# Performance work log

Hardware: AMD Instinct MI355X
Metric: run time of the kernel (lower is better)

The kernel has to match this reference:

```python
import jax, jax.numpy as jnp
import numpy as np

N, C, H, W = 8, 256, 100, 252
TOPK_RATIO = 0.1
CLUSTER_RATIO = 0.125
KNN_K = 10


def setup_inputs() -> dict:
    key = jax.random.key(0)
    ks = jax.random.split(key, 4)
    x = jax.random.normal(ks[0], (N, C, H, W), jnp.float32)
    w1 = jax.random.normal(ks[1], (C, C), jnp.float32) * (1.0 / np.sqrt(C))
    b1 = jnp.zeros((C,), jnp.float32)
    w2 = jax.random.normal(ks[2], (C,), jnp.float32) * (1.0 / np.sqrt(C))
    b2 = jnp.zeros((1,), jnp.float32)
    dis_priority = jnp.ones((N, H, W), jnp.float32)
    record_len = jnp.array([4, 4], dtype=jnp.int32)
    return {"x": x, "w1": w1, "b1": b1, "w2": w2, "b2": b2,
            "dis_priority": dis_priority, "record_len": record_len}


def _layernorm(t, eps=1e-5):
    mu = jnp.mean(t, -1, keepdims=True)
    var = jnp.var(t, -1, keepdims=True)
    return (t - mu) / jnp.sqrt(var + eps)


def reference(x, w1, b1, w2, b2, dis_priority, record_len):
    HW = H * W
    S = int(HW * TOPK_RATIO)                       # sampled tokens per CAV
    K = max(int(np.ceil(S * CLUSTER_RATIO)), 1)    # DPC-KNN cluster count

    xf = x.reshape(N, C, HW)
    # SortSampler: 2layer-fc-256 score net (1x1 convs == per-pixel MLP)
    h1 = jax.nn.relu(jnp.einsum('nch,dc->ndh', xf, w1) + b1[None, :, None])
    score = jax.nn.sigmoid(jnp.einsum('nch,c->nh', h1, w2) + b2)   # [N,HW]
    score = score * dis_priority.reshape(N, HW)

    conf_topk, topk_idx = jax.lax.top_k(score, S)  # descending-sort top-k
    tokens = jnp.take_along_axis(xf, topk_idx[:, None, :], axis=2)  # [N,C,S]
    tokens = _layernorm(tokens.transpose(0, 2, 1))                  # [N,S,C]
    tokens = tokens * conf_topk[..., None]

    # --- cluster_dpc_knn (TCFormer-style DPC-KNN) ---
    sq = jnp.sum(tokens * tokens, -1)
    d2 = sq[:, :, None] + sq[:, None, :] - 2.0 * jnp.einsum('bsc,btc->bst', tokens, tokens)
    dist = jnp.sqrt(jnp.maximum(d2, 1e-12)) / np.sqrt(C)            # [N,S,S]
    neg_near, _ = jax.lax.top_k(-dist, KNN_K)                       # k nearest
    density = jnp.exp(-jnp.mean(neg_near * neg_near, -1))
    density = density + jax.random.uniform(jax.random.key(1), density.shape) * 1e-6
    mask = density[:, None, :] > density[:, :, None]
    dist_max = dist.max(axis=(1, 2), keepdims=True)
    parent_dist = jnp.where(mask, dist, dist_max).min(-1)           # [N,S]
    cscore = parent_dist * density
    _, index_down = jax.lax.top_k(cscore, K)                        # [N,K]
    dist_c = jnp.take_along_axis(dist, index_down[:, :, None], axis=1)  # [N,K,S]
    idx_cluster = jnp.argmin(dist_c, axis=1)                        # [N,S]
    bidx = jnp.arange(N)[:, None]
    idx_cluster = idx_cluster.at[bidx, index_down].set(jnp.arange(K)[None, :])

    # --- merge_tokens: confidence-weighted average per cluster ---
    flat_idx = (idx_cluster + jnp.arange(N)[:, None] * K).reshape(-1)
    wgt = conf_topk.reshape(-1)
    all_w = jax.ops.segment_sum(wgt, flat_idx, num_segments=N * K) + 1e-6
    norm_w = (wgt / all_w[flat_idx])[:, None]
    merged = jax.ops.segment_sum(tokens.reshape(-1, C) * norm_w, flat_idx,
                                 num_segments=N * K).reshape(N, K, C)

    # index_points: broadcast cluster token back to its members
    src = jnp.take_along_axis(merged, idx_cluster[..., None], axis=1)  # [N,S,C]

    # scatter sampled tokens into dense spatial grid
    out = jnp.zeros((N, C, HW), x.dtype)
    out = out.at[bidx, :, topk_idx].set(src)       # [N,S] adv idx -> [N,S,C]

    # ego CAV (first in each record group) keeps full-resolution features
    starts = jnp.concatenate([jnp.zeros((1,), jnp.int32),
                              jnp.cumsum(record_len)[:-1].astype(jnp.int32)])
    is_ego = jnp.zeros((N,), bool).at[starts].set(True)
    out = jnp.where(is_ego[:, None, None], xf, out)
    return out.reshape(N, C, H, W)
```

## Files before the change

kernel.cpp:

```cpp
#include <hip/hip_runtime.h>
#include <cstdio>
#include <cstdint>

#define NN  8
#define CCH 256
#define HWP 25200
#define SS  2520
#define KCL 315
#define KNN 10

__device__ __forceinline__ unsigned fmap(float f) {
  unsigned u = __float_as_uint(f);
  return (u & 0x80000000u) ? ~u : (u | 0x80000000u);
}
__device__ __forceinline__ float funmap(unsigned u) {
  unsigned b = (u & 0x80000000u) ? (u & 0x7fffffffu) : ~u;
  return __uint_as_float(b);
}

__global__ __launch_bounds__(256) void k_w1t(const float* __restrict__ w1, float* __restrict__ w1T) {
  __shared__ float tile[32][33];
  const int bx = blockIdx.x * 32, by = blockIdx.y * 32;
  const int tx = threadIdx.x, ty = threadIdx.y;
  for (int r = 0; r < 32; r += 8)
    tile[ty + r][tx] = w1[(by + ty + r) * CCH + bx + tx];
  __syncthreads();
  for (int r = 0; r < 32; r += 8)
    w1T[(bx + ty + r) * CCH + by + tx] = tile[tx][ty + r];
}

__global__ __launch_bounds__(256) void k_score(
    const float* __restrict__ x, const float* __restrict__ w1T,
    const float* __restrict__ b1, const float* __restrict__ w2,
    const float* __restrict__ b2, const float* __restrict__ pri,
    float* __restrict__ scores)
{
  __shared__ float Wl[16 * 256];
  __shared__ float Xl[16 * 64];
  __shared__ float red[64 * 33];
  const int n = blockIdx.y, p0 = blockIdx.x * 64, tid = threadIdx.x;
  const int dt = tid & 31, pt = tid >> 5;
  const int skk = tid >> 4, sq = tid & 15;
  int sgp = p0 + 4 * sq; if (sgp > HWP - 4) sgp = HWP - 4;
  float acc[8][8];
#pragma unroll
  for (int i = 0; i < 8; ++i)
#pragma unroll
    for (int j = 0; j < 8; ++j) acc[i][j] = 0.f;

  float4 wreg[4], xreg;
  {
    const float4* src = (const float4*)w1T;
#pragma unroll
    for (int i = 0; i < 4; ++i) wreg[i] = src[tid + 256 * i];
    xreg = *(const float4*)&x[(size_t)(n * CCH + skk) * HWP + sgp];
  }

  for (int c0 = 0; c0 < CCH; c0 += 16) {
    __syncthreads();
    {
      float4* dst = (float4*)Wl;
#pragma unroll
      for (int i = 0; i < 4; ++i) dst[tid + 256 * i] = wreg[i];
      *(float4*)&Xl[skk * 64 + 4 * sq] = xreg;
    }
    if (c0 + 16 < CCH) {
      const float4* src = (const float4*)(w1T + (size_t)(c0 + 16) * CCH);
#pragma unroll
      for (int i = 0; i < 4; ++i) wreg[i] = src[tid + 256 * i];
      xreg = *(const float4*)&x[(size_t)(n * CCH + c0 + 16 + skk) * HWP + sgp];
    }
    __syncthreads();
#pragma unroll
    for (int kk = 0; kk < 16; ++kk) {
      const float4 w0 = *(const float4*)&Wl[kk * 256 + 4 * dt];
      const float4 w1v = *(const float4*)&Wl[kk * 256 + 128 + 4 * dt];
      const float4 x0 = *(const float4*)&Xl[kk * 64 + 4 * pt];
      const float4 x1 = *(const float4*)&Xl[kk * 64 + 32 + 4 * pt];
      const float a[8] = {w0.x, w0.y, w0.z, w0.w, w1v.x, w1v.y, w1v.z, w1v.w};
      const float b[8] = {x0.x, x0.y, x0.z, x0.w, x1.x, x1.y, x1.z, x1.w};
#pragma unroll
      for (int di = 0; di < 8; ++di)
#pragma unroll
        for (int pj = 0; pj < 8; ++pj) acc[di][pj] += a[di] * b[pj];
    }
  }
  __syncthreads();
  float part[8];
#pragma unroll
  for (int pj = 0; pj < 8; ++pj) part[pj] = 0.f;
#pragma unroll
  for (int di = 0; di < 8; ++di) {
    int d = (di < 4) ? (4 * dt + di) : (128 + 4 * dt + di - 4);
    float bb = b1[d], wv = w2[d];
#pragma unroll
    for (int pj = 0; pj < 8; ++pj) {
      float h = acc[di][pj] + bb; h = h > 0.f ? h : 0.f;
      part[pj] += h * wv;
    }
  }
#pragma unroll
  for (int pj = 0; pj < 8; ++pj) {
    int px = (pj < 4) ? (4 * pt + pj) : (32 + 4 * pt + pj - 4);
    red[px * 33 + dt] = part[pj];
  }
  __syncthreads();
  if (tid < 64) {
    float s = b2[0];
#pragma unroll
    for (int g = 0; g < 32; ++g) s += red[tid * 33 + g];
    float sc = 1.f / (1.f + expf(-s));
    int p = p0 + tid;
    if (p < HWP) scores[n * HWP + p] = sc * pri[n * HWP + p];
  }
}

__device__ __forceinline__ void bitonic4096_desc(unsigned long long* keys, int tid) {
  for (int k = 2; k <= 4096; k <<= 1) {
    for (int j = k >> 1; j > 0; j >>= 1) {
      for (int i = tid; i < 4096; i += 1024) {
        int ixj = i ^ j;
        if (ixj > i) {
          unsigned long long a = keys[i], b = keys[ixj];
          bool up = ((i & k) == 0);
          if ((a < b) == up) { keys[i] = b; keys[ixj] = a; }
        }
      }
      __syncthreads();
    }
  }
}

__global__ __launch_bounds__(1024) void k_topk_sample(
    const float* __restrict__ scores, int* __restrict__ topk_idx, float* __restrict__ conf)
{
  __shared__ unsigned long long keys[4096];
  unsigned* hist = (unsigned*)keys;
  __shared__ unsigned sh_rank, sh_chosen;
  __shared__ int sh_cnt;
  const int n = blockIdx.x;
  const int tid = threadIdx.x;
  const int sub = tid & 15;
  if (tid == 0) sh_rank = SS;
  __syncthreads();
  unsigned prefix = 0, pmask = 0;
  for (int shift = 24; shift >= 0; shift -= 8) {
    for (int b = tid; b < 4096; b += 1024) hist[b] = 0;
    __syncthreads();
    for (int e4 = tid; e4 < HWP / 4; e4 += 1024) {
      float4 v = *(const float4*)&scores[n * HWP + 4 * e4];
      const float vv[4] = {v.x, v.y, v.z, v.w};
#pragma unroll
      for (int j = 0; j < 4; ++j) {
        unsigned u = fmap(vv[j]);
        if ((u & pmask) == prefix) atomicAdd(&hist[(((u >> shift) & 255u) << 4) + sub], 1u);
      }
    }
    __syncthreads();
    if (tid < 256) {
      unsigned s = 0;
#pragma unroll
      for (int j = 0; j < 16; ++j) s += hist[(tid << 4) + j];
      __syncthreads();
      hist[tid << 4] = s;
    } else __syncthreads();
    __syncthreads();
    if (tid == 0) {
      unsigned r = sh_rank, chosen = 0;
      for (int b = 255; b >= 0; --b) {
        unsigned cb = hist[b << 4];
        if (cb < r) r -= cb; else { chosen = (unsigned)b; break; }
      }
      sh_rank = r; sh_chosen = chosen;
    }
    __syncthreads();
    prefix |= sh_chosen << shift;
    pmask  |= 0xFFu << shift;
    __syncthreads();
  }
  const unsigned uT = prefix;
  if (tid == 0) sh_cnt = 0;
  __syncthreads();
  for (int i = tid; i < 4096; i += 1024) keys[i] = 0ULL;
  __syncthreads();
  for (int e4 = tid; e4 < HWP / 4; e4 += 1024) {
    float4 v = *(const float4*)&scores[n * HWP + 4 * e4];
    const float vv[4] = {v.x, v.y, v.z, v.w};
#pragma unroll
    for (int j = 0; j < 4; ++j) {
      unsigned u = fmap(vv[j]);
      if (u >= uT) {
        int s = atomicAdd(&sh_cnt, 1);
        if (s < 4096) keys[s] = ((unsigned long long)u << 32) | (unsigned)(~(unsigned)(4 * e4 + j));
      }
    }
  }
  __syncthreads();
  bitonic4096_desc(keys, tid);
  for (int t = tid; t < SS; t += 1024) {
    unsigned long long kv = keys[t];
    topk_idx[n * SS + t] = (int)(~(unsigned)kv);
    conf[n * SS + t] = funmap((unsigned)(kv >> 32));
  }
}

__device__ __forceinline__ float block_sum256(float v, float* scratch) {
#pragma unroll
  for (int o = 32; o > 0; o >>= 1) v += __shfl_down(v, o);
  int wid = threadIdx.x >> 6, lane = threadIdx.x & 63;
  if (lane == 0) scratch[wid] = v;
  __syncthreads();
  float r = scratch[0] + scratch[1] + scratch[2] + scratch[3];
  __syncthreads();
  return r;
}

__global__ __launch_bounds__(256) void k_gather_ln(
    const float* __restrict__ x, const int* __restrict__ topk_idx,
    const float* __restrict__ conf, float* __restrict__ tokens, float* __restrict__ sq)
{
  __shared__ float scratch[4];
  const int t = blockIdx.x, n = blockIdx.y, c = threadIdx.x;
  const int p = topk_idx[n * SS + t];
  float v = x[(size_t)(n * CCH + c) * HWP + p];
  float mu = block_sum256(v, scratch) * (1.f / CCH);
  float d = v - mu;
  float var = block_sum256(d * d, scratch) * (1.f / CCH);
  float inv = 1.f / sqrtf(var + 1e-5f);
  float tok = d * inv * conf[n * SS + t];
  tokens[(size_t)(n * SS + t) * CCH + c] = tok;
  float s2 = block_sum256(tok * tok, scratch);
  if (c == 0) sq[n * SS + t] = s2;
}

__global__ __launch_bounds__(256) void k_ttrans(
    const float* __restrict__ tokens, float* __restrict__ tokensT)
{
  __shared__ float tile[64][68];
  const int n = blockIdx.z, t0 = blockIdx.x * 64, cc0 = blockIdx.y * 64;
  const int tid = threadIdx.x;
  for (int l = tid; l < 1024; l += 256) {
    int tr = l >> 4, q = l & 15;
    int gt = t0 + tr;
    float4 v = {0.f, 0.f, 0.f, 0.f};
    if (gt < SS) v = *(const float4*)&tokens[(size_t)(n * SS + gt) * CCH + cc0 + 4 * q];
    *(float4*)&tile[tr][4 * q] = v;
  }
  __syncthreads();
  for (int l = tid; l < 1024; l += 256) {
    int cr = l >> 4, q = l & 15;
    int gt = t0 + 4 * q;
    if (gt <= SS - 4) {
      float4 v;
      v.x = tile[4 * q + 0][cr]; v.y = tile[4 * q + 1][cr];
      v.z = tile[4 * q + 2][cr]; v.w = tile[4 * q + 3][cr];
      *(float4*)&tokensT[(size_t)(n * CCH + cc0 + cr) * SS + gt] = v;
    }
  }
}

__global__ __launch_bounds__(256) void k_gram(
    const float* __restrict__ tokensT, const float* __restrict__ sq,
    float* __restrict__ d2, int* __restrict__ d2max)
{
  const int bi = blockIdx.y, bj = blockIdx.x, n = blockIdx.z;
  if (bj < bi) return;
  __shared__ float Al[16 * 128], Bl[16 * 128];
  __shared__ float redm[256];
  const int i0 = bi * 128, j0 = bj * 128, tid = threadIdx.x;
  const int ti = tid & 15, tj = tid >> 4;
  float acc[8][8];
#pragma unroll
  for (int i = 0; i < 8; ++i)
#pragma unroll
    for (int j = 0; j < 8; ++j) acc[i][j] = 0.f;

  float4 areg[2], breg[2];
  auto stage_load = [&](int c0) {
#pragma unroll
    for (int l0 = 0; l0 < 2; ++l0) {
      int l = tid + 256 * l0;
      int kk = l >> 5, q = l & 31;
      size_t srow = (size_t)(n * CCH + c0 + kk) * SS;
      float4 z = {0.f, 0.f, 0.f, 0.f};
      int gi = i0 + 4 * q;
      areg[l0] = (gi <= SS - 4) ? *(const float4*)&tokensT[srow + gi] : z;
      int gj = j0 + 4 * q;
      breg[l0] = (gj <= SS - 4) ? *(const float4*)&tokensT[srow + gj] : z;
    }
  };
  stage_load(0);

  for (int c0 = 0; c0 < CCH; c0 += 16) {
    __syncthreads();
#pragma unroll
    for (int l0 = 0; l0 < 2; ++l0) {
      int l = tid + 256 * l0;
      int kk = l >> 5, q = l & 31;
      *(float4*)&Al[kk * 128 + 4 * q] = areg[l0];
      *(float4*)&Bl[kk * 128 + 4 * q] = breg[l0];
    }
    if (c0 + 16 < CCH) stage_load(c0 + 16);
    __syncthreads();
#pragma unroll
    for (int kk = 0; kk < 16; ++kk) {
      const float4 a0 = *(const float4*)&Al[kk * 128 + 4 * ti];
      const float4 a1 = *(const float4*)&Al[kk * 128 + 64 + 4 * ti];
      const float4 b0 = *(const float4*)&Bl[kk * 128 + 4 * tj];
      const float4 b1 = *(const float4*)&Bl[kk * 128 + 64 + 4 * tj];
      const float a[8] = {a0.x, a0.y, a0.z, a0.w, a1.x, a1.y, a1.z, a1.w};
      const float b[8] = {b0.x, b0.y, b0.z, b0.w, b1.x, b1.y, b1.z, b1.w};
#pragma unroll
      for (int ii = 0; ii < 8; ++ii)
#pragma unroll
        for (int jj = 0; jj < 8; ++jj) acc[ii][jj] += a[ii] * b[jj];
    }
  }
  int gi[8], gj[8];
  float sqi[8], sqj[8];
#pragma unroll
  for (int ii = 0; ii < 8; ++ii) {
    gi[ii] = i0 + ((ii < 4) ? (4 * ti + ii) : (64 + 4 * ti + ii - 4));
    sqi[ii] = (gi[ii] < SS) ? sq[n * SS + gi[ii]] : 0.f;
    gj[ii] = j0 + ((ii < 4) ? (4 * tj + ii) : (64 + 4 * tj + ii - 4));
    sqj[ii] = (gj[ii] < SS) ? sq[n * SS + gj[ii]] : 0.f;
  }
  float outv[8][8];
  float mx = -3e38f;
#pragma unroll
  for (int ii = 0; ii < 8; ++ii)
#pragma unroll
    for (int jj = 0; jj < 8; ++jj) {
      float o = sqi[ii] + sqj[jj] - 2.f * acc[ii][jj];
      outv[ii][jj] = o;
      if (gi[ii] < SS && gj[jj] < SS) mx = fmaxf(mx, o);
    }
#pragma unroll
  for (int ii = 0; ii < 8; ++ii) {
    if (gi[ii] < SS) {
      size_t row = (size_t)(n * SS + gi[ii]) * SS;
      int jb0 = j0 + 4 * tj;
      float4 o0 = {outv[ii][0], outv[ii][1], outv[ii][2], outv[ii][3]};
      *(float4*)&d2[row + jb0] = o0;
      int jb1 = j0 + 64 + 4 * tj;
      if (jb1 < SS) {
        float4 o1 = {outv[ii][4], outv[ii][5], outv[ii][6], outv[ii][7]};
        *(float4*)&d2[row + jb1] = o1;
      }
    }
  }
  if (bi != bj) {
#pragma unroll
    for (int jj = 0; jj < 8; ++jj) {
      if (gj[jj] < SS) {
        size_t row = (size_t)(n * SS + gj[jj]) * SS;
        int ib0 = i0 + 4 * ti;
        float4 m0 = {outv[0][jj], outv[1][jj], outv[2][jj], outv[3][jj]};
        *(float4*)&d2[row + ib0] = m0;
        int ib1 = i0 + 64 + 4 * ti;
        if (ib1 < SS) {
          float4 m1 = {outv[4][jj], outv[5][jj], outv[6][jj], outv[7][jj]};
          *(float4*)&d2[row + ib1] = m1;
        }
      }
    }
  }
  redm[tid] = mx; __syncthreads();
  for (int s = 128; s > 0; s >>= 1) {
    if (tid < s) redm[tid] = fmaxf(redm[tid], redm[tid + s]);
    __syncthreads();
  }
  if (tid == 0) atomicMax(&d2max[n], __float_as_int(redm[0]));
}

__global__ __launch_bounds__(256) void k_knn(
    const float* __restrict__ d2, float* __restrict__ density)
{
  const int n = blockIdx.y;
  const int w = threadIdx.x >> 6, lane = threadIdx.x & 63;
  const int i = blockIdx.x * 4 + w;
  const float* dr = &d2[(size_t)(n * SS + i) * SS];
  float s[KNN];
#pragma unroll
  for (int k = 0; k < KNN; ++k) s[k] = 3e38f;
  for (int e = lane; e < SS; e += 64) {
    float t = dr[e];
#pragma unroll
    for (int k = 0; k < KNN; ++k) {
      float lo = fminf(s[k], t);
      t = fmaxf(s[k], t);
      s[k] = lo;
    }
  }
  float sum = 0.f;
  for (int r = 0; r < KNN; ++r) {
    float m = s[0];
#pragma unroll
    for (int o = 32; o > 0; o >>= 1) m = fminf(m, __shfl_xor(m, o));
    unsigned long long msk = __ballot(s[0] == m);
    int first = __ffsll(msk) - 1;
    if (lane == first) {
#pragma unroll
      for (int k = 0; k < KNN - 1; ++k) s[k] = s[k + 1];
      s[KNN - 1] = 3e38f;
    }
    sum += fmaxf(m, 1e-12f);
  }
  if (lane == 0) density[n * SS + i] = expf(-sum * (1.f / (KNN * CCH)));
}

__global__ __launch_bounds__(256) void k_parent(
    const float* __restrict__ d2, const float* __restrict__ density,
    const int* __restrict__ d2max, float* __restrict__ cscore)
{
  __shared__ float swv[4];
  const int i = blockIdx.x, n = blockIdx.y, tid = threadIdx.x;
  const float di = density[n * SS + i];
  const float* dr = &d2[(size_t)(n * SS + i) * SS];
  float m = 3e38f;
  for (int e = tid; e < SS; e += 256) {
    float dj = density[n * SS + e];
    float v = dr[e];
    if (dj > di && v < m) m = v;
  }
#pragma unroll
  for (int o = 32; o > 0; o >>= 1) m = fminf(m, __shfl_down(m, o));
  int wid = tid >> 6, lane = tid & 63;
  if (lane == 0) swv[wid] = m;
  __syncthreads();
  if (tid == 0) {
    float mm = fminf(fminf(swv[0], swv[1]), fminf(swv[2], swv[3]));
    mm = fminf(mm, __int_as_float(d2max[n]));
    float pd = sqrtf(fmaxf(mm, 1e-12f)) * 0.0625f;
    cscore[n * SS + i] = pd * di;
  }
}

__global__ __launch_bounds__(1024) void k_topk_centers(
    const float* __restrict__ cscore, int* __restrict__ index_down)
{
  __shared__ unsigned long long keys[4096];
  const int n = blockIdx.x, tid = threadIdx.x;
  for (int i = tid; i < 4096; i += 1024) {
    unsigned long long kv = 0ULL;
    if (i < SS) kv = ((unsigned long long)fmap(cscore[n * SS + i]) << 32) | (unsigned)(~(unsigned)i);
    keys[i] = kv;
  }
  __syncthreads();
  bitonic4096_desc(keys, tid);
  for (int t = tid; t < KCL; t += 1024)
    index_down[n * KCL + t] = (int)(~(unsigned)keys[t]);
}

__global__ __launch_bounds__(256) void k_assign(
    const float* __restrict__ d2, const int* __restrict__ index_down,
    int* __restrict__ idx_cluster)
{
  const int n = blockIdx.y;
  const int i = blockIdx.x * 256 + threadIdx.x;
  if (i >= SS) return;
  float best = 3e38f; int bk = 0;
  for (int k = 0; k < KCL; ++k) {
    int r = index_down[n * KCL + k];
    float v = d2[(size_t)(n * SS + r) * SS + i];
    if (v < best) { best = v; bk = k; }
  }
  idx_cluster[n * SS + i] = bk;
}

__global__ void k_center_overwrite(const int* __restrict__ index_down, int* __restrict__ idx_cluster) {
  const int n = blockIdx.x; const int k = threadIdx.x;
  if (k < KCL) idx_cluster[n * SS + index_down[n * KCL + k]] = k;
}

__global__ __launch_bounds__(256) void k_weights(
    const int* __restrict__ idx_cluster, const float* __restrict__ conf, float* __restrict__ all_w)
{
  const int n = blockIdx.y; const int i = blockIdx.x * 256 + threadIdx.x;
  if (i >= SS) return;
  atomicAdd(&all_w[n * KCL + idx_cluster[n * SS + i]], conf[n * SS + i]);
}

__global__ __launch_bounds__(256) void k_merge(
    const int* __restrict__ idx_cluster, const float* __restrict__ conf,
    const float* __restrict__ all_w, const float* __restrict__ tokens, float* __restrict__ merged)
{
  const int t = blockIdx.x, n = blockIdx.y, c = threadIdx.x;
  const int k = idx_cluster[n * SS + t];
  const float w = conf[n * SS + t] / (all_w[n * KCL + k] + 1e-6f);
  atomicAdd(&merged[(size_t)(n * KCL + k) * CCH + c],
            tokens[(size_t)(n * SS + t) * CCH + c] * w);
}

__global__ __launch_bounds__(256) void k_kmap(
    const int* __restrict__ topk_idx, const int* __restrict__ idx_cluster, int* __restrict__ kmap)
{
  const int n = blockIdx.y; const int i = blockIdx.x * 256 + threadIdx.x;
  if (i >= SS) return;
  kmap[n * HWP + topk_idx[n * SS + i]] = idx_cluster[n * SS + i];
}

__global__ void k_ego(const int* __restrict__ record_len, int R, int* __restrict__ ego) {
  if (threadIdx.x == 0 && blockIdx.x == 0) {
    int acc = 0;
    for (int r = 0; r < R; ++r) {
      if (acc >= 0 && acc < NN) ego[acc] = 1;
      acc += record_len[r];
    }
  }
}

__global__ __launch_bounds__(256) void k_output(
    const float* __restrict__ x, const float* __restrict__ merged,
    const int* __restrict__ kmap, const int* __restrict__ ego, float* __restrict__ out)
{
  const int n = blockIdx.z;
  const int cg = blockIdx.y * 16;
  const int p4 = blockIdx.x * 256 + threadIdx.x;
  if (p4 >= HWP / 4) return;
  const size_t pbase = 4 * (size_t)p4;
  if (ego[n]) {
#pragma unroll 4
    for (int c = cg; c < cg + 16; ++c) {
      const size_t base = (size_t)(n * CCH + c) * HWP + pbase;
      *(float4*)&out[base] = *(const float4*)&x[base];
    }
  } else {
    const int4 k4 = *(const int4*)&kmap[n * HWP + pbase];
    const float* mb = &merged[(size_t)n * KCL * CCH];
#pragma unroll 4
    for (int c = cg; c < cg + 16; ++c) {
      float4 v;
      v.x = (k4.x >= 0) ? mb[k4.x * CCH + c] : 0.f;
      v.y = (k4.y >= 0) ? mb[k4.y * CCH + c] : 0.f;
      v.z = (k4.z >= 0) ? mb[k4.z * CCH + c] : 0.f;
      v.w = (k4.w >= 0) ? mb[k4.w * CCH + c] : 0.f;
      *(float4*)&out[(size_t)(n * CCH + c) * HWP + pbase] = v;
    }
  }
}

extern "C" void kernel_launch(void* const* d_in, const int* in_sizes, int n_in,
                              void* d_out, int out_size, void* d_ws, size_t ws_size,
                              hipStream_t stream)
{
  const float* x   = (const float*)d_in[0];
  const float* w1  = (const float*)d_in[1];
  const float* b1  = (const float*)d_in[2];
  const float* w2  = (const float*)d_in[3];
  const float* b2  = (const float*)d_in[4];
  const float* pri = (const float*)d_in[5];
  const int*   rec = (const int*)d_in[6];
  const int R = in_sizes[6];
  float* out = (float*)d_out;

  char* ws = (char*)d_ws;
  size_t off = 0;
  auto alloc = [&](size_t bytes) -> char* {
    char* p = ws + off;
    off = (off + bytes + 255) & ~(size_t)255;
    return p;
  };
  float* scores      = (float*)alloc(sizeof(float) * NN * HWP);
  int*   topk_idx    = (int*)  alloc(sizeof(int)   * NN * SS);
  float* conf        = (float*)alloc(sizeof(float) * NN * SS);
  float* tokens      = (float*)alloc(sizeof(float) * (size_t)NN * SS * CCH);
  float* tokensT     = (float*)alloc(sizeof(float) * (size_t)NN * CCH * SS);
  float* w1T         = (float*)alloc(sizeof(float) * CCH * CCH);
  float* sq          = (float*)alloc(sizeof(float) * NN * SS);
  float* density     = (float*)alloc(sizeof(float) * NN * SS);
  float* cscore      = (float*)alloc(sizeof(float) * NN * SS);
  int*   d2max       = (int*)  alloc(sizeof(int)   * NN);
  int*   index_down  = (int*)  alloc(sizeof(int)   * NN * KCL);
  int*   idx_cluster = (int*)  alloc(sizeof(int)   * NN * SS);
  float* all_w       = (float*)alloc(sizeof(float) * NN * KCL);
  float* merged      = (float*)alloc(sizeof(float) * (size_t)NN * KCL * CCH);
  int*   kmap        = (int*)  alloc(sizeof(int)   * NN * HWP);
  int*   ego         = (int*)  alloc(sizeof(int)   * NN);
  float* d2          = (float*)alloc(sizeof(float) * (size_t)NN * SS * SS);
  if (off > ws_size)
    fprintf(stderr, "ERMVP kernel: workspace too small: need %zu, have %zu\n", off, ws_size);

  hipMemsetAsync(d2max, 0, sizeof(int) * NN, stream);
  hipMemsetAsync(all_w, 0, sizeof(float) * NN * KCL, stream);
  hipMemsetAsync(merged, 0, sizeof(float) * (size_t)NN * KCL * CCH, stream);
  hipMemsetAsync(kmap, 0xFF, sizeof(int) * NN * HWP, stream);
  hipMemsetAsync(ego, 0, sizeof(int) * NN, stream);

  k_w1t<<<dim3(8, 8), dim3(32, 8), 0, stream>>>(w1, w1T);
  k_score<<<dim3((HWP + 63) / 64, NN), 256, 0, stream>>>(x, w1T, b1, w2, b2, pri, scores);
  k_topk_sample<<<NN, 1024, 0, stream>>>(scores, topk_idx, conf);
  k_gather_ln<<<dim3(SS, NN), 256, 0, stream>>>(x, topk_idx, conf, tokens, sq);
  k_ttrans<<<dim3((SS + 63) / 64, CCH / 64, NN), 256, 0, stream>>>(tokens, tokensT);
  k_gram<<<dim3(20, 20, NN), 256, 0, stream>>>(tokensT, sq, d2, d2max);
  k_knn<<<dim3(SS / 4, NN), 256, 0, stream>>>(d2, density);
  k_parent<<<dim3(SS, NN), 256, 0, stream>>>(d2, density, d2max, cscore);
  k_topk_centers<<<NN, 1024, 0, stream>>>(cscore, index_down);
  k_assign<<<dim3((SS + 255) / 256, NN), 256, 0, stream>>>(d2, index_down, idx_cluster);
  k_center_overwrite<<<NN, 320, 0, stream>>>(index_down, idx_cluster);
  k_weights<<<dim3((SS + 255) / 256, NN), 256, 0, stream>>>(idx_cluster, conf, all_w);
  k_merge<<<dim3(SS, NN), 256, 0, stream>>>(idx_cluster, conf, all_w, tokens, merged);
  k_kmap<<<dim3((SS + 255) / 256, NN), 256, 0, stream>>>(topk_idx, idx_cluster, kmap);
  k_ego<<<1, 64, 0, stream>>>(rec, R, ego);
  k_output<<<dim3((HWP / 4 + 255) / 256, (CCH + 15) / 16, NN), 256, 0, stream>>>(x, merged, kmap, ego, out);
}
```

Before: 1.405 ms.

## Use direct global-to-LDS double-buffered loads in score and gram GEMMs, split assign

The score MLP and Gram-matrix GEMMs now stage tiles with global_load_lds straight into double-buffered shared memory instead of going through registers, and set an occupancy hint of 3 blocks. The aim is to cut register pressure and drop one barrier per k-step. Cluster assignment splits the 315 centers across 4 waves and reduces packed (distance, index) keys, giving more parallelism per column. The kmap scatter is fused into the weights kernel, removing one launch. One risk: the loop keeps a single barrier while reading one buffer and writing the other, and nothing explicitly waits for the async LDS loads before they are read.

After: 1.785 ms. +27.0%, slower.

```diff
diff --git a/kernel.cpp b/kernel.cpp
--- a/kernel.cpp
+++ b/kernel.cpp
@@ -18,6 +18,12 @@
   return __uint_as_float(b);
 }
 
+__device__ __forceinline__ void gl16(const float* g, float* lds_wave_base) {
+  __builtin_amdgcn_global_load_lds(
+      (const __attribute__((address_space(1))) void*)g,
+      (__attribute__((address_space(3))) void*)lds_wave_base, 16, 0, 0);
+}
+
 __global__ __launch_bounds__(256) void k_w1t(const float* __restrict__ w1, float* __restrict__ w1T) {
   __shared__ float tile[32][33];
   const int bx = blockIdx.x * 32, by = blockIdx.y * 32;
@@ -29,54 +35,46 @@
     w1T[(bx + ty + r) * CCH + by + tx] = tile[tx][ty + r];
 }
 
-__global__ __launch_bounds__(256) void k_score(
+__global__ __launch_bounds__(256, 3) void k_score(
     const float* __restrict__ x, const float* __restrict__ w1T,
     const float* __restrict__ b1, const float* __restrict__ w2,
     const float* __restrict__ b2, const float* __restrict__ pri,
     float* __restrict__ scores)
 {
-  __shared__ float Wl[16 * 256];
-  __shared__ float Xl[16 * 64];
+  __shared__ float Wl[2][16 * 256];
+  __shared__ float Xl[2][16 * 64];
   __shared__ float red[64 * 33];
   const int n = blockIdx.y, p0 = blockIdx.x * 64, tid = threadIdx.x;
   const int dt = tid & 31, pt = tid >> 5;
+  const int wb = tid & ~63;
   const int skk = tid >> 4, sq = tid & 15;
   int sgp = p0 + 4 * sq; if (sgp > HWP - 4) sgp = HWP - 4;
+
   float acc[8][8];
 #pragma unroll
   for (int i = 0; i < 8; ++i)
 #pragma unroll
     for (int j = 0; j < 8; ++j) acc[i][j] = 0.f;
 
-  float4 wreg[4], xreg;
-  {
-    const float4* src = (const float4*)w1T;
-#pragma unroll
-    for (int i = 0; i < 4; ++i) wreg[i] = src[tid + 256 * i];
-    xreg = *(const float4*)&x[(size_t)(n * CCH + skk) * HWP + sgp];
-  }
-
-  for (int c0 = 0; c0 < CCH; c0 += 16) {
-    __syncthreads();
-    {
-      float4* dst = (float4*)Wl;
-#pragma unroll
-      for (int i = 0; i < 4; ++i) dst[tid + 256 * i] = wreg[i];
-      *(float4*)&Xl[skk * 64 + 4 * sq] = xreg;
-    }
-    if (c0 + 16 < CCH) {
-      const float4* src = (const float4*)(w1T + (size_t)(c0 + 16) * CCH);
-#pragma unroll
-      for (int i = 0; i < 4; ++i) wreg[i] = src[tid + 256 * i];
-      xreg = *(const float4*)&x[(size_t)(n * CCH + c0 + 16 + skk) * HWP + sgp];
-    }
-    __syncthreads();
+  auto stage = [&](int buf, int c0) {
+    const float* wsrc = w1T + (size_t)c0 * CCH;
+#pragma unroll
+    for (int i = 0; i < 4; ++i)
+      gl16(wsrc + 4 * (i * 256 + tid), &Wl[buf][(i * 256 + wb) * 4]);
+    gl16(&x[(size_t)(n * CCH + c0 + skk) * HWP + sgp], &Xl[buf][wb * 4]);
+  };
+
+  stage(0, 0);
+  for (int t = 0; t < 16; ++t) {
+    const int buf = t & 1;
+    __syncthreads();
+    if (t + 1 < 16) stage(buf ^ 1, 16 * (t + 1));
 #pragma unroll
     for (int kk = 0; kk < 16; ++kk) {
-      const float4 w0 = *(const float4*)&Wl[kk * 256 + 4 * dt];
-      const float4 w1v = *(const float4*)&Wl[kk * 256 + 128 + 4 * dt];
-      const float4 x0 = *(const float4*)&Xl[kk * 64 + 4 * pt];
-      const float4 x1 = *(const float4*)&Xl[kk * 64 + 32 + 4 * pt];
+      const float4 w0 = *(const float4*)&Wl[buf][kk * 256 + 4 * dt];
+      const float4 w1v = *(const float4*)&Wl[buf][kk * 256 + 128 + 4 * dt];
+      const float4 x0 = *(const float4*)&Xl[buf][kk * 64 + 4 * pt];
+      const float4 x1 = *(const float4*)&Xl[buf][kk * 64 + 32 + 4 * pt];
       const float a[8] = {w0.x, w0.y, w0.z, w0.w, w1v.x, w1v.y, w1v.z, w1v.w};
       const float b[8] = {x0.x, x0.y, x0.z, x0.w, x1.x, x1.y, x1.z, x1.w};
 #pragma unroll
@@ -259,13 +257,13 @@
   }
 }
 
-__global__ __launch_bounds__(256) void k_gram(
+__global__ __launch_bounds__(256, 3) void k_gram(
     const float* __restrict__ tokensT, const float* __restrict__ sq,
     float* __restrict__ d2, int* __restrict__ d2max)
 {
   const int bi = blockIdx.y, bj = blockIdx.x, n = blockIdx.z;
   if (bj < bi) return;
-  __shared__ float Al[16 * 128], Bl[16 * 128];
+  __shared__ float Al[2][16 * 128], Bl[2][16 * 128];
   __shared__ float redm[256];
   const int i0 = bi * 128, j0 = bj * 128, tid = threadIdx.x;
   const int ti = tid & 15, tj = tid >> 4;
@@ -275,39 +273,31 @@
 #pragma unroll
     for (int j = 0; j < 8; ++j) acc[i][j] = 0.f;
 
-  float4 areg[2], breg[2];
-  auto stage_load = [&](int c0) {
+  auto stage = [&](int buf, int c0) {
 #pragma unroll
     for (int l0 = 0; l0 < 2; ++l0) {
       int l = tid + 256 * l0;
       int kk = l >> 5, q = l & 31;
       size_t srow = (size_t)(n * CCH + c0 + kk) * SS;
-      float4 z = {0.f, 0.f, 0.f, 0.f};
-      int gi = i0 + 4 * q;
-      areg[l0] = (gi <= SS - 4) ? *(const float4*)&tokensT[srow + gi] : z;
-      int gj = j0 + 4 * q;
-      breg[l0] = (gj <= SS - 4) ? *(const float4*)&tokensT[srow + gj] : z;
+      int gi = i0 + 4 * q; if (gi > SS - 4) gi = SS - 4;
+      int gj = j0 + 4 * q; if (gj > SS - 4) gj = SS - 4;
+      int lbase = (l & ~63) * 4;
+      gl16(&tokensT[srow + gi], &Al[buf][lbase]);
+      gl16(&tokensT[srow + gj], &Bl[buf][lbase]);
     }
   };
-  stage_load(0);
-
-  for (int c0 = 0; c0 < CCH; c0 += 16) {
-    __syncthreads();
-#pragma unroll
-    for (int l0 = 0; l0 < 2; ++l0) {
-      int l = tid + 256 * l0;
-      int kk = l >> 5, q = l & 31;
-      *(float4*)&Al[kk * 128 + 4 * q] = areg[l0];
-      *(float4*)&Bl[kk * 128 + 4 * q] = breg[l0];
-    }
-    if (c0 + 16 < CCH) stage_load(c0 + 16);
-    __syncthreads();
+
+  stage(0, 0);
+  for (int t = 0; t < 16; ++t) {
+    const int buf = t & 1;
+    __syncthreads();
+    if (t + 1 < 16) stage(buf ^ 1, 16 * (t + 1));
 #pragma unroll
     for (int kk = 0; kk < 16; ++kk) {
-      const float4 a0 = *(const float4*)&Al[kk * 128 + 4 * ti];
-      const float4 a1 = *(const float4*)&Al[kk * 128 + 64 + 4 * ti];
-      const float4 b0 = *(const float4*)&Bl[kk * 128 + 4 * tj];
-      const float4 b1 = *(const float4*)&Bl[kk * 128 + 64 + 4 * tj];
+      const float4 a0 = *(const float4*)&Al[buf][kk * 128 + 4 * ti];
+      const float4 a1 = *(const float4*)&Al[buf][kk * 128 + 64 + 4 * ti];
+      const float4 b0 = *(const float4*)&Bl[buf][kk * 128 + 4 * tj];
+      const float4 b1 = *(const float4*)&Bl[buf][kk * 128 + 64 + 4 * tj];
       const float a[8] = {a0.x, a0.y, a0.z, a0.w, a1.x, a1.y, a1.z, a1.w};
       const float b[8] = {b0.x, b0.y, b0.z, b0.w, b1.x, b1.y, b1.z, b1.w};
 #pragma unroll
@@ -456,16 +446,29 @@
     const float* __restrict__ d2, const int* __restrict__ index_down,
     int* __restrict__ idx_cluster)
 {
+  __shared__ unsigned long long best[4][64];
   const int n = blockIdx.y;
-  const int i = blockIdx.x * 256 + threadIdx.x;
-  if (i >= SS) return;
-  float best = 3e38f; int bk = 0;
-  for (int k = 0; k < KCL; ++k) {
-    int r = index_down[n * KCL + k];
-    float v = d2[(size_t)(n * SS + r) * SS + i];
-    if (v < best) { best = v; bk = k; }
-  }
-  idx_cluster[n * SS + i] = bk;
+  const int lane = threadIdx.x & 63, w = threadIdx.x >> 6;
+  const int i = blockIdx.x * 64 + lane;
+  const int kc = (KCL + 3) / 4;
+  const int k0 = w * kc, k1 = (k0 + kc < KCL) ? (k0 + kc) : KCL;
+  unsigned long long bp = ~0ULL;
+  if (i < SS) {
+    for (int k = k0; k < k1; ++k) {
+      int r = index_down[n * KCL + k];
+      float v = d2[(size_t)(n * SS + r) * SS + i];
+      unsigned long long p = ((unsigned long long)fmap(v) << 32) | (unsigned)k;
+      bp = (p < bp) ? p : bp;
+    }
+  }
+  best[w][lane] = bp;
+  __syncthreads();
+  if (w == 0 && i < SS) {
+    unsigned long long b = best[0][lane];
+#pragma unroll
+    for (int ww = 1; ww < 4; ++ww) { unsigned long long o = best[ww][lane]; b = (o < b) ? o : b; }
+    idx_cluster[n * SS + i] = (int)(unsigned)(b & 0xFFFFFFFFu);
+  }
 }
 
 __global__ void k_center_overwrite(const int* __restrict__ index_down, int* __restrict__ idx_cluster) {
@@ -473,12 +476,15 @@
   if (k < KCL) idx_cluster[n * SS + index_down[n * KCL + k]] = k;
 }
 
-__global__ __launch_bounds__(256) void k_weights(
-    const int* __restrict__ idx_cluster, const float* __restrict__ conf, float* __restrict__ all_w)
+__global__ __launch_bounds__(256) void k_wk(
+    const int* __restrict__ idx_cluster, const float* __restrict__ conf,
+    const int* __restrict__ topk_idx, float* __restrict__ all_w, int* __restrict__ kmap)
 {
   const int n = blockIdx.y; const int i = blockIdx.x * 256 + threadIdx.x;
   if (i >= SS) return;
-  atomicAdd(&all_w[n * KCL + idx_cluster[n * SS + i]], conf[n * SS + i]);
+  const int k = idx_cluster[n * SS + i];
+  atomicAdd(&all_w[n * KCL + k], conf[n * SS + i]);
+  kmap[n * HWP + topk_idx[n * SS + i]] = k;
 }
 
 __global__ __launch_bounds__(256) void k_merge(
@@ -490,14 +496,6 @@
   const float w = conf[n * SS + t] / (all_w[n * KCL + k] + 1e-6f);
   atomicAdd(&merged[(size_t)(n * KCL + k) * CCH + c],
             tokens[(size_t)(n * SS + t) * CCH + c] * w);
-}
-
-__global__ __launch_bounds__(256) void k_kmap(
-    const int* __restrict__ topk_idx, const int* __restrict__ idx_cluster, int* __restrict__ kmap)
-{
-  const int n = blockIdx.y; const int i = blockIdx.x * 256 + threadIdx.x;
-  if (i >= SS) return;
-  kmap[n * HWP + topk_idx[n * SS + i]] = idx_cluster[n * SS + i];
 }
 
 __global__ void k_ego(const int* __restrict__ record_len, int R, int* __restrict__ ego) {
@@ -596,11 +594,10 @@
   k_knn<<<dim3(SS / 4, NN), 256, 0, stream>>>(d2, density);
   k_parent<<<dim3(SS, NN), 256, 0, stream>>>(d2, density, d2max, cscore);
   k_topk_centers<<<NN, 1024, 0, stream>>>(cscore, index_down);
-  k_assign<<<dim3((SS + 255) / 256, NN), 256, 0, stream>>>(d2, index_down, idx_cluster);
+  k_assign<<<dim3((SS + 63) / 64, NN), 256, 0, stream>>>(d2, index_down, idx_cluster);
   k_center_overwrite<<<NN, 320, 0, stream>>>(index_down, idx_cluster);
-  k_weights<<<dim3((SS + 255) / 256, NN), 256, 0, stream>>>(idx_cluster, conf, all_w);
+  k_wk<<<dim3((SS + 255) / 256, NN), 256, 0, stream>>>(idx_cluster, conf, topk_idx, all_w, kmap);
   k_merge<<<dim3(SS, NN), 256, 0, stream>>>(idx_cluster, conf, all_w, tokens, merged);
-  k_kmap<<<dim3((SS + 255) / 256, NN), 256, 0, stream>>>(topk_idx, idx_cluster, kmap);
   k_ego<<<1, 64, 0, stream>>>(rec, R, ego);
   k_output<<<dim3((HWP / 4 + 255) / 256, (CCH + 15) / 16, NN), 256, 0, stream>>>(x, merged, kmap, ego, out);
 }
```
